# Kernel optimization log

Hardware: AMD Instinct MI355X
Metric: run time of the kernel (lower is better)

Reference implementation:

```python
import jax, jax.numpy as jnp
import numpy as np

N_USER = 100000
N_ITEM = 200000


def setup_inputs() -> dict:
    key = jax.random.key(0)
    ks = jax.random.split(key, 9)
    n = N_USER + N_ITEM
    nnz = 9600000
    return {
        "users_emb": jax.random.normal(ks[0], (N_USER, 64), dtype=jnp.float32) * 0.1,
        "items_emb": jax.random.normal(ks[1], (N_ITEM, 64), dtype=jnp.float32) * 0.1,
        "user_sim_neighbor": jax.random.randint(ks[2], (N_USER, 10), 0, N_USER),
        "user_sim_weight": jax.random.uniform(ks[3], (N_USER, 10), dtype=jnp.float32),
        "item_sim_neighbor": jax.random.randint(ks[4], (N_ITEM, 10), 0, N_ITEM),
        "item_sim_weight": jax.random.uniform(ks[5], (N_ITEM, 10), dtype=jnp.float32),
        "graph_rows": jax.random.randint(ks[6], (nnz,), 0, n),
        "graph_cols": jax.random.randint(ks[7], (nnz,), 0, n),
        "graph_vals": jax.random.uniform(ks[8], (nnz,), dtype=jnp.float32),
    }


def reference(users_emb, items_emb, user_sim_neighbor, user_sim_weight,
              item_sim_neighbor, item_sim_weight, graph_rows, graph_cols, graph_vals):
    n = users_emb.shape[0] + items_emb.shape[0]
    emb = jnp.concatenate([users_emb, items_emb], axis=0)  # [n, d]

    # top-k neighbor gather + weighted sum (users then items)
    user_neighbor_emb = jnp.einsum("nk,nkd->nd", user_sim_weight, users_emb[user_sim_neighbor])
    item_neighbor_emb = jnp.einsum("nk,nkd->nd", item_sim_weight, items_emb[item_sim_neighbor])
    neighbor_emb = jnp.concatenate([user_neighbor_emb, item_neighbor_emb], axis=0)

    # sparse graph matmul: all_emb = Graph @ emb  (COO rows/cols/vals)
    all_emb = jax.ops.segment_sum(graph_vals[:, None] * emb[graph_cols], graph_rows,
                                  num_segments=n)

    emb = emb + neighbor_emb + all_emb
    users = emb[:users_emb.shape[0]]
    items = emb[users_emb.shape[0]:]
    return users, items
```

## Files before the change

kernel.cpp:

```cpp
#include <hip/hip_runtime.h>

#define N_USER 100000
#define N_ITEM 200000
#define N_TOT  (N_USER + N_ITEM)
#define D      64
#define RPB    64
#define NB     ((N_TOT + RPB - 1) / RPB)
#define NBLK_F 512
#define THR_A  512
#define CAP    2304
#define SCAN_CHUNK 2048

__device__ __forceinline__ unsigned short f2bf(float f) {
    unsigned b = __float_as_uint(f);
    unsigned r = (b + 0x7FFFu + ((b >> 16) & 1u)) >> 16;
    return (unsigned short)r;
}
__device__ __forceinline__ float bf2f(unsigned short u) {
    return __uint_as_float(((unsigned)u) << 16);
}

__global__ __launch_bounds__(256) void conv_kernel(const float* __restrict__ users,
                                                   const float* __restrict__ items,
                                                   ushort* __restrict__ emb16) {
    size_t i = (size_t)blockIdx.x * blockDim.x + threadIdx.x;
    const size_t total = (size_t)N_TOT * D / 4;
    if (i >= total) return;
    size_t e0 = i * 4;
    const size_t usz = (size_t)N_USER * D;
    const float* src = (e0 < usz) ? users + e0 : items + (e0 - usz);
    float4 v = *reinterpret_cast<const float4*>(src);
    ushort4 o;
    o.x = f2bf(v.x); o.y = f2bf(v.y); o.z = f2bf(v.z); o.w = f2bf(v.w);
    *reinterpret_cast<ushort4*>(emb16 + e0) = o;
}


__global__ __launch_bounds__(THR_A) void count_fused(const int* __restrict__ rows,
                                                     int* __restrict__ tot, int nnz, int chunk) {
    __shared__ int h[NB];
    for (int k = threadIdx.x; k < NB; k += blockDim.x) h[k] = 0;
    __syncthreads();
    int lo = blockIdx.x * chunk;
    int hi = min(lo + chunk, nnz);
    for (int i = lo + threadIdx.x; i < hi; i += blockDim.x)
        atomicAdd(&h[rows[i] >> 6], 1);
    __syncthreads();
    for (int k = threadIdx.x; k < NB; k += blockDim.x)
        if (h[k]) atomicAdd(&tot[k], h[k]);
}

__global__ __launch_bounds__(1024) void scan_kernel(const int* __restrict__ tot,
                                                    int* __restrict__ bstart,
                                                    int* __restrict__ gcur, int nnz) {
    __shared__ int s[1024];
    const int t = threadIdx.x;
    const int PER = (NB + 1023) / 1024;
    int loc[8];
    int sum = 0;
    #pragma unroll
    for (int k = 0; k < PER; ++k) {
        int idx = t * PER + k;
        int v = (idx < NB) ? tot[idx] : 0;
        loc[k] = sum; sum += v;
    }
    s[t] = sum;
    __syncthreads();
    for (int off = 1; off < 1024; off <<= 1) {
        int v = (t >= off) ? s[t - off] : 0;
        __syncthreads();
        s[t] += v;
        __syncthreads();
    }
    int base = s[t] - sum;
    #pragma unroll
    for (int k = 0; k < PER; ++k) {
        int idx = t * PER + k;
        if (idx < NB) { bstart[idx] = base + loc[k]; gcur[idx] = base + loc[k]; }
    }
    if (t == 1023) bstart[NB] = nnz;
}

__global__ __launch_bounds__(THR_A) void fill_fused(const int* __restrict__ rows,
                                                    const int* __restrict__ cols,
                                                    const float* __restrict__ vals,
                                                    int* __restrict__ gcur,
                                                    uint2* __restrict__ eg, int nnz, int chunk) {
    __shared__ int h[NB];
    for (int k = threadIdx.x; k < NB; k += blockDim.x) h[k] = 0;
    __syncthreads();
    int lo = blockIdx.x * chunk;
    int hi = min(lo + chunk, nnz);
    for (int i = lo + threadIdx.x; i < hi; i += blockDim.x)
        atomicAdd(&h[rows[i] >> 6], 1);
    __syncthreads();
    for (int k = threadIdx.x; k < NB; k += blockDim.x)
        if (h[k]) h[k] = atomicAdd(&gcur[k], h[k]);
    __syncthreads();
    for (int i = lo + threadIdx.x; i < hi; i += blockDim.x) {
        int r = rows[i];
        int k = r >> 6;
        int slot = atomicAdd(&h[k], 1);
        uint2 p;
        p.x = ((unsigned)(r & 63) << 19) | (unsigned)cols[i];
        p.y = __float_as_uint(vals[i]);
        eg[slot] = p;
    }
}

__global__ __launch_bounds__(256) void sortgather_kernel(
    const ushort* __restrict__ emb16,
    const int*   __restrict__ unb,   const float* __restrict__ uw,
    const int*   __restrict__ inb,   const float* __restrict__ iw,
    const int*   __restrict__ bstart, const uint2* __restrict__ eg,
    float* __restrict__ out)
{
    __shared__ uint2 lds_e[CAP];
    __shared__ int h[RPB], st[RPB], cur[RPB];

    const int tid  = threadIdx.x;
    const int g    = tid >> 4;
    const int sub  = tid & 15;
    const int d0   = sub * 4;
    const int k    = blockIdx.x;
    const int row0 = k * RPB;

    float4 acc[4];
    #pragma unroll
    for (int rr = 0; rr < 4; ++rr) {
        const int row = row0 + rr * 16 + g;
        if (row >= N_TOT) { acc[rr] = make_float4(0.f, 0.f, 0.f, 0.f); continue; }
        ushort4 ub = *reinterpret_cast<const ushort4*>(emb16 + (size_t)row * D + d0);
        float4 a = make_float4(bf2f(ub.x), bf2f(ub.y), bf2f(ub.z), bf2f(ub.w));
        if (row < N_USER) {
            const int*   nb = unb + (size_t)row * 10;
            const float* w  = uw  + (size_t)row * 10;
            #pragma unroll
            for (int q = 0; q < 10; ++q) {
                ushort4 u = *reinterpret_cast<const ushort4*>(emb16 + (size_t)nb[q] * D + d0);
                float wq = w[q];
                a.x += wq * bf2f(u.x); a.y += wq * bf2f(u.y);
                a.z += wq * bf2f(u.z); a.w += wq * bf2f(u.w);
            }
        } else {
            const int r = row - N_USER;
            const int*   nb = inb + (size_t)r * 10;
            const float* w  = iw  + (size_t)r * 10;
            #pragma unroll
            for (int q = 0; q < 10; ++q) {
                ushort4 u = *reinterpret_cast<const ushort4*>(emb16 + ((size_t)nb[q] + N_USER) * D + d0);
                float wq = w[q];
                a.x += wq * bf2f(u.x); a.y += wq * bf2f(u.y);
                a.z += wq * bf2f(u.z); a.w += wq * bf2f(u.w);
            }
        }
        acc[rr] = a;
    }

    const int s = bstart[k];
    const int e = bstart[k + 1];

    for (int cs = s; cs < e; cs += CAP) {
        const int n = min(e - cs, CAP);

        if (tid < RPB) h[tid] = 0;
        __syncthreads();
        for (int i = tid; i < n; i += 256)
            atomicAdd(&h[eg[cs + i].x >> 19], 1);
        __syncthreads();
        if (tid < RPB) {
            int orig = h[tid];
            int v = orig;
            #pragma unroll
            for (int off = 1; off < RPB; off <<= 1) {
                int u = __shfl_up(v, off);
                if (tid >= off) v += u;
            }
            st[tid]  = v - orig;
            cur[tid] = v - orig;
        }
        __syncthreads();
        for (int i = tid; i < n; i += 256) {
            uint2 p = eg[cs + i];
            int slot = atomicAdd(&cur[p.x >> 19], 1);
            lds_e[slot] = p;
        }
        __syncthreads();

        #pragma unroll
        for (int rr = 0; rr < 4; ++rr) {
            const int r  = rr * 16 + g;
            const int b0 = st[r];
            const int cr = h[r];
            int j = 0;
            for (; j + 3 < cr; j += 4) {
                uint2 p0 = lds_e[b0 + j],     p1 = lds_e[b0 + j + 1];
                uint2 p2 = lds_e[b0 + j + 2], p3 = lds_e[b0 + j + 3];
                ushort4 u0 = *reinterpret_cast<const ushort4*>(emb16 + (size_t)(p0.x & 0x7FFFFu) * D + d0);
                ushort4 u1 = *reinterpret_cast<const ushort4*>(emb16 + (size_t)(p1.x & 0x7FFFFu) * D + d0);
                ushort4 u2 = *reinterpret_cast<const ushort4*>(emb16 + (size_t)(p2.x & 0x7FFFFu) * D + d0);
                ushort4 u3 = *reinterpret_cast<const ushort4*>(emb16 + (size_t)(p3.x & 0x7FFFFu) * D + d0);
                float a0 = __uint_as_float(p0.y), a1 = __uint_as_float(p1.y);
                float a2 = __uint_as_float(p2.y), a3 = __uint_as_float(p3.y);
                acc[rr].x += a0 * bf2f(u0.x); acc[rr].y += a0 * bf2f(u0.y);
                acc[rr].z += a0 * bf2f(u0.z); acc[rr].w += a0 * bf2f(u0.w);
                acc[rr].x += a1 * bf2f(u1.x); acc[rr].y += a1 * bf2f(u1.y);
                acc[rr].z += a1 * bf2f(u1.z); acc[rr].w += a1 * bf2f(u1.w);
                acc[rr].x += a2 * bf2f(u2.x); acc[rr].y += a2 * bf2f(u2.y);
                acc[rr].z += a2 * bf2f(u2.z); acc[rr].w += a2 * bf2f(u2.w);
                acc[rr].x += a3 * bf2f(u3.x); acc[rr].y += a3 * bf2f(u3.y);
                acc[rr].z += a3 * bf2f(u3.z); acc[rr].w += a3 * bf2f(u3.w);
            }
            for (; j < cr; ++j) {
                uint2 p = lds_e[b0 + j];
                ushort4 u = *reinterpret_cast<const ushort4*>(emb16 + (size_t)(p.x & 0x7FFFFu) * D + d0);
                float a = __uint_as_float(p.y);
                acc[rr].x += a * bf2f(u.x); acc[rr].y += a * bf2f(u.y);
                acc[rr].z += a * bf2f(u.z); acc[rr].w += a * bf2f(u.w);
            }
        }
        __syncthreads();
    }

    #pragma unroll
    for (int rr = 0; rr < 4; ++rr) {
        const int row = row0 + rr * 16 + g;
        if (row < N_TOT)
            *reinterpret_cast<float4*>(&out[(size_t)row * D + d0]) = acc[rr];
    }
}


__global__ void count_kernel(const int* __restrict__ rows, int* __restrict__ cnt, int nnz) {
    int i = blockIdx.x * blockDim.x + threadIdx.x;
    int stride = gridDim.x * blockDim.x;
    for (; i < nnz; i += stride) atomicAdd(&cnt[rows[i]], 1);
}

__global__ void scan_block_sums(const int* __restrict__ cnt, int* __restrict__ bsum, int n) {
    __shared__ int sdata[256];
    int base = blockIdx.x * SCAN_CHUNK;
    int s = 0;
    for (int t = threadIdx.x; t < SCAN_CHUNK; t += 256) {
        int idx = base + t;
        s += (idx < n) ? cnt[idx] : 0;
    }
    sdata[threadIdx.x] = s;
    __syncthreads();
    for (int off = 128; off > 0; off >>= 1) {
        if (threadIdx.x < off) sdata[threadIdx.x] += sdata[threadIdx.x + off];
        __syncthreads();
    }
    if (threadIdx.x == 0) bsum[blockIdx.x] = sdata[0];
}

__global__ void scan_bsum_kernel(int* __restrict__ bsum, int nb) {
    if (threadIdx.x == 0 && blockIdx.x == 0) {
        int acc = 0;
        for (int i = 0; i < nb; ++i) { int v = bsum[i]; bsum[i] = acc; acc += v; }
    }
}

__global__ void scan_final(const int* __restrict__ cnt, const int* __restrict__ bsum,
                           int* __restrict__ row_start, int n, int nnz) {
    __shared__ int sums[256];
    int b = blockIdx.x, t = threadIdx.x;
    int base = b * SCAN_CHUNK;
    int loc[8];
    int s = 0;
    #pragma unroll
    for (int k = 0; k < 8; ++k) {
        int idx = base + t * 8 + k;
        int v = (idx < n) ? cnt[idx] : 0;
        loc[k] = s; s += v;
    }
    sums[t] = s;
    __syncthreads();
    for (int off = 1; off < 256; off <<= 1) {
        int v = (t >= off) ? sums[t - off] : 0;
        __syncthreads();
        sums[t] += v;
        __syncthreads();
    }
    int off0 = bsum[b] + (sums[t] - s);
    #pragma unroll
    for (int k = 0; k < 8; ++k) {
        int idx = base + t * 8 + k;
        if (idx < n) row_start[idx] = off0 + loc[k];
    }
    if (b == gridDim.x - 1 && t == 255) row_start[n] = nnz;
}

__global__ void fill_kernel(const int* __restrict__ rows, const int* __restrict__ cols,
                            const float* __restrict__ vals, const int* __restrict__ row_start,
                            int* __restrict__ pos, uint2* __restrict__ eg, int nnz) {
    int i = blockIdx.x * blockDim.x + threadIdx.x;
    int stride = gridDim.x * blockDim.x;
    for (; i < nnz; i += stride) {
        int r = rows[i];
        int p = atomicAdd(&pos[r], 1);
        uint2 e;
        e.x = (unsigned)cols[i];
        e.y = __float_as_uint(vals[i]);
        eg[row_start[r] + p] = e;
    }
}

__global__ __launch_bounds__(256) void gather16_kernel(
    const float* __restrict__ users, const float* __restrict__ items,
    const int*   __restrict__ unb,   const float* __restrict__ uw,
    const int*   __restrict__ inb,   const float* __restrict__ iw,
    const int*   __restrict__ row_start, const uint2* __restrict__ eg,
    float* __restrict__ out)
{
    const int tid = threadIdx.x;
    const int grp = tid >> 4;
    const int sub = tid & 15;
    const int row = blockIdx.x * 16 + grp;
    if (row >= N_TOT) return;
    const int d0 = sub * 4;

    float4 acc;
    if (row < N_USER) {
        acc = *reinterpret_cast<const float4*>(&users[(size_t)row * D + d0]);
        const int*   nb = unb + (size_t)row * 10;
        const float* w  = uw  + (size_t)row * 10;
        #pragma unroll
        for (int q = 0; q < 10; ++q) {
            float4 v = *reinterpret_cast<const float4*>(&users[(size_t)nb[q] * D + d0]);
            float wq = w[q];
            acc.x += wq * v.x; acc.y += wq * v.y; acc.z += wq * v.z; acc.w += wq * v.w;
        }
    } else {
        int r = row - N_USER;
        acc = *reinterpret_cast<const float4*>(&items[(size_t)r * D + d0]);
        const int*   nb = inb + (size_t)r * 10;
        const float* w  = iw  + (size_t)r * 10;
        #pragma unroll
        for (int q = 0; q < 10; ++q) {
            float4 v = *reinterpret_cast<const float4*>(&items[(size_t)nb[q] * D + d0]);
            float wq = w[q];
            acc.x += wq * v.x; acc.y += wq * v.y; acc.z += wq * v.z; acc.w += wq * v.w;
        }
    }

    const int s = row_start[row];
    const int e = row_start[row + 1];
    int i = s;
    for (; i + 3 < e; i += 4) {
        uint2 p0 = eg[i], p1 = eg[i + 1], p2 = eg[i + 2], p3 = eg[i + 3];
        int c0 = (int)(p0.x & 0x7FFFFu), c1 = (int)(p1.x & 0x7FFFFu);
        int c2 = (int)(p2.x & 0x7FFFFu), c3 = (int)(p3.x & 0x7FFFFu);
        const float* s0 = (c0 < N_USER) ? users + (size_t)c0 * D : items + (size_t)(c0 - N_USER) * D;
        const float* s1 = (c1 < N_USER) ? users + (size_t)c1 * D : items + (size_t)(c1 - N_USER) * D;
        const float* s2 = (c2 < N_USER) ? users + (size_t)c2 * D : items + (size_t)(c2 - N_USER) * D;
        const float* s3 = (c3 < N_USER) ? users + (size_t)c3 * D : items + (size_t)(c3 - N_USER) * D;
        float4 v0 = *reinterpret_cast<const float4*>(s0 + d0);
        float4 v1 = *reinterpret_cast<const float4*>(s1 + d0);
        float4 v2 = *reinterpret_cast<const float4*>(s2 + d0);
        float4 v3 = *reinterpret_cast<const float4*>(s3 + d0);
        float a0 = __uint_as_float(p0.y), a1 = __uint_as_float(p1.y);
        float a2 = __uint_as_float(p2.y), a3 = __uint_as_float(p3.y);
        acc.x += a0 * v0.x; acc.y += a0 * v0.y; acc.z += a0 * v0.z; acc.w += a0 * v0.w;
        acc.x += a1 * v1.x; acc.y += a1 * v1.y; acc.z += a1 * v1.z; acc.w += a1 * v1.w;
        acc.x += a2 * v2.x; acc.y += a2 * v2.y; acc.z += a2 * v2.z; acc.w += a2 * v2.w;
        acc.x += a3 * v3.x; acc.y += a3 * v3.y; acc.z += a3 * v3.z; acc.w += a3 * v3.w;
    }
    for (; i < e; ++i) {
        uint2 p = eg[i];
        int c = (int)(p.x & 0x7FFFFu);
        const float* src = (c < N_USER) ? users + (size_t)c * D : items + (size_t)(c - N_USER) * D;
        float4 v = *reinterpret_cast<const float4*>(src + d0);
        float a = __uint_as_float(p.y);
        acc.x += a * v.x; acc.y += a * v.y; acc.z += a * v.z; acc.w += a * v.w;
    }

    *reinterpret_cast<float4*>(&out[(size_t)row * D + d0]) = acc;
}

__global__ __launch_bounds__(256) void base_neighbor_kernel(
    const float* __restrict__ users, const float* __restrict__ items,
    const int*   __restrict__ unb,   const float* __restrict__ uw,
    const int*   __restrict__ inb,   const float* __restrict__ iw,
    float* __restrict__ out)
{
    int gtid = blockIdx.x * blockDim.x + threadIdx.x;
    int row  = gtid >> 6;
    int lane = gtid & 63;
    if (row >= N_TOT) return;
    float acc;
    if (row < N_USER) {
        acc = users[(size_t)row * D + lane];
        const int*   nb = unb + (size_t)row * 10;
        const float* w  = uw  + (size_t)row * 10;
        #pragma unroll
        for (int q = 0; q < 10; ++q) acc += w[q] * users[(size_t)nb[q] * D + lane];
    } else {
        int r = row - N_USER;
        acc = items[(size_t)r * D + lane];
        const int*   nb = inb + (size_t)r * 10;
        const float* w  = iw  + (size_t)r * 10;
        #pragma unroll
        for (int q = 0; q < 10; ++q) acc += w[q] * items[(size_t)nb[q] * D + lane];
    }
    out[(size_t)row * D + lane] = acc;
}

__global__ __launch_bounds__(256) void edge_scatter_kernel(
    const float* __restrict__ users, const float* __restrict__ items,
    const int*   __restrict__ rows,  const int* __restrict__ cols,
    const float* __restrict__ vals,
    float* __restrict__ out, int nnz)
{
    int gtid = blockIdx.x * blockDim.x + threadIdx.x;
    int e    = gtid >> 6;
    int lane = gtid & 63;
    if (e >= nnz) return;
    int   r = rows[e];
    int   c = cols[e];
    float v = vals[e];
    const float* src = (c < N_USER) ? (users + (size_t)c * D)
                                    : (items + (size_t)(c - N_USER) * D);
    atomicAdd(&out[(size_t)r * D + lane], v * src[lane]);
}

extern "C" void kernel_launch(void* const* d_in, const int* in_sizes, int n_in,
                              void* d_out, int out_size, void* d_ws, size_t ws_size,
                              hipStream_t stream) {
    const float* users = (const float*)d_in[0];
    const float* items = (const float*)d_in[1];
    const int*   unb   = (const int*)  d_in[2];
    const float* uw    = (const float*)d_in[3];
    const int*   inb   = (const int*)  d_in[4];
    const float* iw    = (const float*)d_in[5];
    const int*   grow  = (const int*)  d_in[6];
    const int*   gcol  = (const int*)  d_in[7];
    const float* gval  = (const float*)d_in[8];
    float* out = (float*)d_out;

    const int nnz = in_sizes[6];

    const size_t A = 255;
    const size_t sz_eg       = (((size_t)nnz * 8) + A) & ~A;
    const size_t sz_tot      = (((size_t)NB * 4) + A) & ~A;
    const size_t sz_bstart   = (((size_t)(NB + 1) * 4) + A) & ~A;
    const size_t sz_gcur     = (((size_t)NB * 4) + A) & ~A;
    const size_t sz_rowstart = (((size_t)(N_TOT + 1) * 4) + A) & ~A;
    const size_t sz_emb16    = (((size_t)N_TOT * D * 2) + A) & ~A;
    const size_t need0 = sz_eg + sz_tot + sz_bstart + sz_gcur + sz_emb16;

    const size_t sz_cnt  = (((size_t)N_TOT * 4) + A) & ~A;
    const int    nb2     = (N_TOT + SCAN_CHUNK - 1) / SCAN_CHUNK;
    const size_t sz_bsum = (((size_t)nb2 * 4) + A) & ~A;
    const size_t need2 = sz_eg + sz_rowstart + sz_cnt + sz_bsum;

    if (ws_size >= need0) {
        char* wsp = (char*)d_ws;
        uint2*  eg     = (uint2*)wsp;  wsp += sz_eg;
        int*    tot    = (int*)wsp;    wsp += sz_tot;
        int*    bstart = (int*)wsp;    wsp += sz_bstart;
        int*    gcur   = (int*)wsp;    wsp += sz_gcur;
        ushort* emb16  = (ushort*)wsp;

        const int chunk = (nnz + NBLK_F - 1) / NBLK_F;
        const int conv_grid = (int)(((size_t)N_TOT * D / 4 + 255) / 256);

        conv_kernel<<<conv_grid, 256, 0, stream>>>(users, items, emb16);
        hipMemsetAsync(tot, 0, (size_t)NB * 4, stream);
        count_fused<<<NBLK_F, THR_A, 0, stream>>>(grow, tot, nnz, chunk);
        scan_kernel<<<1, 1024, 0, stream>>>(tot, bstart, gcur, nnz);
        fill_fused<<<NBLK_F, THR_A, 0, stream>>>(grow, gcol, gval, gcur, eg, nnz, chunk);
        sortgather_kernel<<<NB, 256, 0, stream>>>(emb16, unb, uw, inb, iw,
                                                  bstart, eg, out);
    } else if (ws_size >= need2) {
        char* wsp = (char*)d_ws;
        uint2* eg        = (uint2*)wsp;  wsp += sz_eg;
        int*   row_start = (int*)wsp;    wsp += sz_rowstart;
        int*   cnt       = (int*)wsp;    wsp += sz_cnt;
        int*   bsum      = (int*)wsp;

        hipMemsetAsync(cnt, 0, (size_t)N_TOT * 4, stream);
        count_kernel<<<2048, 256, 0, stream>>>(grow, cnt, nnz);
        scan_block_sums<<<nb2, 256, 0, stream>>>(cnt, bsum, N_TOT);
        scan_bsum_kernel<<<1, 64, 0, stream>>>(bsum, nb2);
        scan_final<<<nb2, 256, 0, stream>>>(cnt, bsum, row_start, N_TOT, nnz);
        hipMemsetAsync(cnt, 0, (size_t)N_TOT * 4, stream);
        fill_kernel<<<2048, 256, 0, stream>>>(grow, gcol, gval, row_start, cnt, eg, nnz);
        const int g16_grid = (N_TOT + 15) / 16;
        gather16_kernel<<<g16_grid, 256, 0, stream>>>(users, items, unb, uw, inb, iw,
                                                      row_start, eg, out);
    } else {
        int grid = (int)(((long long)N_TOT * 64 + 255) / 256);
        base_neighbor_kernel<<<grid, 256, 0, stream>>>(users, items, unb, uw, inb, iw, out);
        long long ethreads = (long long)nnz * 64;
        long long egrid = (ethreads + 255) / 256;
        edge_scatter_kernel<<<(int)egrid, 256, 0, stream>>>(users, items, grow, gcol, gval, out, nnz);
    }
}
```

Baseline: 571.6 us.

## Replace global count/scan/fill with per-block local binning and segmented gather

Removes the global histogram, single-block scan, and global-atomic fill pass. Each of 256 partition blocks now bins its own chunk of edges locally and writes a per-block offset table S. The gather kernel then has each of its 256 threads read one partition's segment for that row block. This drops one full pass over rows plus the memset and scan launches. In exchange the gather reads are strided and serial per thread, and edges beyond CAP2 per row block are silently dropped instead of being processed in chunks, which risks wrong results if a block exceeds capacity.

```diff
diff --git a/kernel.cpp b/kernel.cpp
--- a/kernel.cpp
+++ b/kernel.cpp
@@ -6,9 +6,8 @@
 #define D      64
 #define RPB    64
 #define NB     ((N_TOT + RPB - 1) / RPB)
-#define NBLK_F 512
-#define THR_A  512
-#define CAP    2304
+#define NBLK_L 256
+#define CAP2   2560
 #define SCAN_CHUNK 2048
 
 __device__ __forceinline__ unsigned short f2bf(float f) {
@@ -35,76 +34,62 @@
     *reinterpret_cast<ushort4*>(emb16 + e0) = o;
 }
 
-
-__global__ __launch_bounds__(THR_A) void count_fused(const int* __restrict__ rows,
-                                                     int* __restrict__ tot, int nnz, int chunk) {
-    __shared__ int h[NB];
-    for (int k = threadIdx.x; k < NB; k += blockDim.x) h[k] = 0;
-    __syncthreads();
-    int lo = blockIdx.x * chunk;
-    int hi = min(lo + chunk, nnz);
-    for (int i = lo + threadIdx.x; i < hi; i += blockDim.x)
+__global__ __launch_bounds__(512) void local_bin(const int* __restrict__ rows,
+                                                 const int* __restrict__ cols,
+                                                 const float* __restrict__ vals,
+                                                 int* __restrict__ S,
+                                                 uint2* __restrict__ eg, int nnz, int chunk) {
+    __shared__ int h[NB + 1];
+    __shared__ int ps[512];
+    const int b   = blockIdx.x;
+    const int tid = threadIdx.x;
+    const int lo  = b * chunk;
+    const int hi  = min(lo + chunk, nnz);
+
+    for (int k = tid; k < NB + 1; k += 512) h[k] = 0;
+    __syncthreads();
+    for (int i = lo + tid; i < hi; i += 512)
         atomicAdd(&h[rows[i] >> 6], 1);
     __syncthreads();
-    for (int k = threadIdx.x; k < NB; k += blockDim.x)
-        if (h[k]) atomicAdd(&tot[k], h[k]);
-}
-
-__global__ __launch_bounds__(1024) void scan_kernel(const int* __restrict__ tot,
-                                                    int* __restrict__ bstart,
-                                                    int* __restrict__ gcur, int nnz) {
-    __shared__ int s[1024];
-    const int t = threadIdx.x;
-    const int PER = (NB + 1023) / 1024;
-    int loc[8];
+
+    const int SEG = (NB + 511) / 512;
+    int loc[10];
     int sum = 0;
     #pragma unroll
-    for (int k = 0; k < PER; ++k) {
-        int idx = t * PER + k;
-        int v = (idx < NB) ? tot[idx] : 0;
-        loc[k] = sum; sum += v;
-    }
-    s[t] = sum;
-    __syncthreads();
-    for (int off = 1; off < 1024; off <<= 1) {
-        int v = (t >= off) ? s[t - off] : 0;
+    for (int j = 0; j < SEG; ++j) {
+        int idx = tid * SEG + j;
+        int v = (idx < NB) ? h[idx] : 0;
+        loc[j] = sum; sum += v;
+    }
+    ps[tid] = sum;
+    __syncthreads();
+    for (int off = 1; off < 512; off <<= 1) {
+        int v = (tid >= off) ? ps[tid - off] : 0;
         __syncthreads();
-        s[t] += v;
+        ps[tid] += v;
         __syncthreads();
     }
-    int base = s[t] - sum;
-    #pragma unroll
-    for (int k = 0; k < PER; ++k) {
-        int idx = t * PER + k;
-        if (idx < NB) { bstart[idx] = base + loc[k]; gcur[idx] = base + loc[k]; }
-    }
-    if (t == 1023) bstart[NB] = nnz;
-}
-
-__global__ __launch_bounds__(THR_A) void fill_fused(const int* __restrict__ rows,
-                                                    const int* __restrict__ cols,
-                                                    const float* __restrict__ vals,
-                                                    int* __restrict__ gcur,
-                                                    uint2* __restrict__ eg, int nnz, int chunk) {
-    __shared__ int h[NB];
-    for (int k = threadIdx.x; k < NB; k += blockDim.x) h[k] = 0;
-    __syncthreads();
-    int lo = blockIdx.x * chunk;
-    int hi = min(lo + chunk, nnz);
-    for (int i = lo + threadIdx.x; i < hi; i += blockDim.x)
-        atomicAdd(&h[rows[i] >> 6], 1);
-    __syncthreads();
-    for (int k = threadIdx.x; k < NB; k += blockDim.x)
-        if (h[k]) h[k] = atomicAdd(&gcur[k], h[k]);
-    __syncthreads();
-    for (int i = lo + threadIdx.x; i < hi; i += blockDim.x) {
+    const int myb = ps[tid] - sum;
+    __syncthreads();
+    #pragma unroll
+    for (int j = 0; j < SEG; ++j) {
+        int idx = tid * SEG + j;
+        if (idx < NB) h[idx] = myb + loc[j];
+    }
+    if (tid == 511) h[NB] = myb + sum;
+    __syncthreads();
+
+    for (int k = tid; k < NB + 1; k += 512)
+        S[(size_t)b * (NB + 1) + k] = h[k];
+    __syncthreads();
+
+    for (int i = lo + tid; i < hi; i += 512) {
         int r = rows[i];
-        int k = r >> 6;
-        int slot = atomicAdd(&h[k], 1);
+        int slot = atomicAdd(&h[r >> 6], 1);
         uint2 p;
         p.x = ((unsigned)(r & 63) << 19) | (unsigned)cols[i];
         p.y = __float_as_uint(vals[i]);
-        eg[slot] = p;
+        eg[lo + slot] = p;
     }
 }
 
@@ -112,10 +97,10 @@
     const ushort* __restrict__ emb16,
     const int*   __restrict__ unb,   const float* __restrict__ uw,
     const int*   __restrict__ inb,   const float* __restrict__ iw,
-    const int*   __restrict__ bstart, const uint2* __restrict__ eg,
-    float* __restrict__ out)
+    const int*   __restrict__ S,     const uint2* __restrict__ eg,
+    float* __restrict__ out, int chunk)
 {
-    __shared__ uint2 lds_e[CAP];
+    __shared__ uint2 lds_e[CAP2];
     __shared__ int h[RPB], st[RPB], cur[RPB];
 
     const int tid  = threadIdx.x;
@@ -124,6 +109,16 @@
     const int d0   = sub * 4;
     const int k    = blockIdx.x;
     const int row0 = k * RPB;
+
+    const size_t sidx = (size_t)tid * (NB + 1) + k;
+    const int rs = S[sidx];
+    const int re = S[sidx + 1];
+    const size_t cbase = (size_t)tid * chunk;
+
+    if (tid < RPB) h[tid] = 0;
+    __syncthreads();
+    for (int i = rs; i < re; ++i)
+        atomicAdd(&h[eg[cbase + i].x >> 19], 1);
 
     float4 acc[4];
     #pragma unroll
@@ -156,70 +151,59 @@
         }
         acc[rr] = a;
     }
-
-    const int s = bstart[k];
-    const int e = bstart[k + 1];
-
-    for (int cs = s; cs < e; cs += CAP) {
-        const int n = min(e - cs, CAP);
-
-        if (tid < RPB) h[tid] = 0;
-        __syncthreads();
-        for (int i = tid; i < n; i += 256)
-            atomicAdd(&h[eg[cs + i].x >> 19], 1);
-        __syncthreads();
-        if (tid < RPB) {
-            int orig = h[tid];
-            int v = orig;
-            #pragma unroll
-            for (int off = 1; off < RPB; off <<= 1) {
-                int u = __shfl_up(v, off);
-                if (tid >= off) v += u;
-            }
-            st[tid]  = v - orig;
-            cur[tid] = v - orig;
-        }
-        __syncthreads();
-        for (int i = tid; i < n; i += 256) {
-            uint2 p = eg[cs + i];
-            int slot = atomicAdd(&cur[p.x >> 19], 1);
-            lds_e[slot] = p;
-        }
-        __syncthreads();
-
+    __syncthreads();
+
+    if (tid < RPB) {
+        int orig = h[tid];
+        int v = orig;
         #pragma unroll
-        for (int rr = 0; rr < 4; ++rr) {
-            const int r  = rr * 16 + g;
-            const int b0 = st[r];
-            const int cr = h[r];
-            int j = 0;
-            for (; j + 3 < cr; j += 4) {
-                uint2 p0 = lds_e[b0 + j],     p1 = lds_e[b0 + j + 1];
-                uint2 p2 = lds_e[b0 + j + 2], p3 = lds_e[b0 + j + 3];
-                ushort4 u0 = *reinterpret_cast<const ushort4*>(emb16 + (size_t)(p0.x & 0x7FFFFu) * D + d0);
-                ushort4 u1 = *reinterpret_cast<const ushort4*>(emb16 + (size_t)(p1.x & 0x7FFFFu) * D + d0);
-                ushort4 u2 = *reinterpret_cast<const ushort4*>(emb16 + (size_t)(p2.x & 0x7FFFFu) * D + d0);
-                ushort4 u3 = *reinterpret_cast<const ushort4*>(emb16 + (size_t)(p3.x & 0x7FFFFu) * D + d0);
-                float a0 = __uint_as_float(p0.y), a1 = __uint_as_float(p1.y);
-                float a2 = __uint_as_float(p2.y), a3 = __uint_as_float(p3.y);
-                acc[rr].x += a0 * bf2f(u0.x); acc[rr].y += a0 * bf2f(u0.y);
-                acc[rr].z += a0 * bf2f(u0.z); acc[rr].w += a0 * bf2f(u0.w);
-                acc[rr].x += a1 * bf2f(u1.x); acc[rr].y += a1 * bf2f(u1.y);
-                acc[rr].z += a1 * bf2f(u1.z); acc[rr].w += a1 * bf2f(u1.w);
-                acc[rr].x += a2 * bf2f(u2.x); acc[rr].y += a2 * bf2f(u2.y);
-                acc[rr].z += a2 * bf2f(u2.z); acc[rr].w += a2 * bf2f(u2.w);
-                acc[rr].x += a3 * bf2f(u3.x); acc[rr].y += a3 * bf2f(u3.y);
-                acc[rr].z += a3 * bf2f(u3.z); acc[rr].w += a3 * bf2f(u3.w);
-            }
-            for (; j < cr; ++j) {
-                uint2 p = lds_e[b0 + j];
-                ushort4 u = *reinterpret_cast<const ushort4*>(emb16 + (size_t)(p.x & 0x7FFFFu) * D + d0);
-                float a = __uint_as_float(p.y);
-                acc[rr].x += a * bf2f(u.x); acc[rr].y += a * bf2f(u.y);
-                acc[rr].z += a * bf2f(u.z); acc[rr].w += a * bf2f(u.w);
-            }
-        }
-        __syncthreads();
+        for (int off = 1; off < RPB; off <<= 1) {
+            int u = __shfl_up(v, off);
+            if (tid >= off) v += u;
+        }
+        st[tid]  = v - orig;
+        cur[tid] = v - orig;
+    }
+    __syncthreads();
+
+    for (int i = rs; i < re; ++i) {
+        uint2 p = eg[cbase + i];
+        int slot = atomicAdd(&cur[p.x >> 19], 1);
+        if (slot < CAP2) lds_e[slot] = p;
+    }
+    __syncthreads();
+
+    #pragma unroll
+    for (int rr = 0; rr < 4; ++rr) {
+        const int r  = rr * 16 + g;
+        const int b0 = st[r];
+        const int cr = h[r];
+        int j = 0;
+        for (; j + 3 < cr; j += 4) {
+            uint2 p0 = lds_e[b0 + j],     p1 = lds_e[b0 + j + 1];
+            uint2 p2 = lds_e[b0 + j + 2], p3 = lds_e[b0 + j + 3];
+            ushort4 u0 = *reinterpret_cast<const ushort4*>(emb16 + (size_t)(p0.x & 0x7FFFFu) * D + d0);
+            ushort4 u1 = *reinterpret_cast<const ushort4*>(emb16 + (size_t)(p1.x & 0x7FFFFu) * D + d0);
+            ushort4 u2 = *reinterpret_cast<const ushort4*>(emb16 + (size_t)(p2.x & 0x7FFFFu) * D + d0);
+            ushort4 u3 = *reinterpret_cast<const ushort4*>(emb16 + (size_t)(p3.x & 0x7FFFFu) * D + d0);
+            float a0 = __uint_as_float(p0.y), a1 = __uint_as_float(p1.y);
+            float a2 = __uint_as_float(p2.y), a3 = __uint_as_float(p3.y);
+            acc[rr].x += a0 * bf2f(u0.x); acc[rr].y += a0 * bf2f(u0.y);
+            acc[rr].z += a0 * bf2f(u0.z); acc[rr].w += a0 * bf2f(u0.w);
+            acc[rr].x += a1 * bf2f(u1.x); acc[rr].y += a1 * bf2f(u1.y);
+            acc[rr].z += a1 * bf2f(u1.z); acc[rr].w += a1 * bf2f(u1.w);
+            acc[rr].x += a2 * bf2f(u2.x); acc[rr].y += a2 * bf2f(u2.y);
+            acc[rr].z += a2 * bf2f(u2.z); acc[rr].w += a2 * bf2f(u2.w);
+            acc[rr].x += a3 * bf2f(u3.x); acc[rr].y += a3 * bf2f(u3.y);
+            acc[rr].z += a3 * bf2f(u3.z); acc[rr].w += a3 * bf2f(u3.w);
+        }
+        for (; j < cr; ++j) {
+            uint2 p = lds_e[b0 + j];
+            ushort4 u = *reinterpret_cast<const ushort4*>(emb16 + (size_t)(p.x & 0x7FFFFu) * D + d0);
+            float a = __uint_as_float(p.y);
+            acc[rr].x += a * bf2f(u.x); acc[rr].y += a * bf2f(u.y);
+            acc[rr].z += a * bf2f(u.z); acc[rr].w += a * bf2f(u.w);
+        }
     }
 
     #pragma unroll
@@ -442,12 +426,10 @@
 
     const size_t A = 255;
     const size_t sz_eg       = (((size_t)nnz * 8) + A) & ~A;
-    const size_t sz_tot      = (((size_t)NB * 4) + A) & ~A;
-    const size_t sz_bstart   = (((size_t)(NB + 1) * 4) + A) & ~A;
-    const size_t sz_gcur     = (((size_t)NB * 4) + A) & ~A;
+    const size_t sz_S        = (((size_t)NBLK_L * (NB + 1) * 4) + A) & ~A;
+    const size_t sz_emb16    = (((size_t)N_TOT * D * 2) + A) & ~A;
     const size_t sz_rowstart = (((size_t)(N_TOT + 1) * 4) + A) & ~A;
-    const size_t sz_emb16    = (((size_t)N_TOT * D * 2) + A) & ~A;
-    const size_t need0 = sz_eg + sz_tot + sz_bstart + sz_gcur + sz_emb16;
+    const size_t need0 = sz_eg + sz_S + sz_emb16;
 
     const size_t sz_cnt  = (((size_t)N_TOT * 4) + A) & ~A;
     const int    nb2     = (N_TOT + SCAN_CHUNK - 1) / SCAN_CHUNK;
@@ -456,22 +438,17 @@
 
     if (ws_size >= need0) {
         char* wsp = (char*)d_ws;
-        uint2*  eg     = (uint2*)wsp;  wsp += sz_eg;
-        int*    tot    = (int*)wsp;    wsp += sz_tot;
-        int*    bstart = (int*)wsp;    wsp += sz_bstart;
-        int*    gcur   = (int*)wsp;    wsp += sz_gcur;
-        ushort* emb16  = (ushort*)wsp;
-
-        const int chunk = (nnz + NBLK_F - 1) / NBLK_F;
+        uint2*  eg    = (uint2*)wsp;  wsp += sz_eg;
+        int*    S     = (int*)wsp;    wsp += sz_S;
+        ushort* emb16 = (ushort*)wsp;
+
+        const int chunk = (nnz + NBLK_L - 1) / NBLK_L;
         const int conv_grid = (int)(((size_t)N_TOT * D / 4 + 255) / 256);
 
         conv_kernel<<<conv_grid, 256, 0, stream>>>(users, items, emb16);
-        hipMemsetAsync(tot, 0, (size_t)NB * 4, stream);
-        count_fused<<<NBLK_F, THR_A, 0, stream>>>(grow, tot, nnz, chunk);
-        scan_kernel<<<1, 1024, 0, stream>>>(tot, bstart, gcur, nnz);
-        fill_fused<<<NBLK_F, THR_A, 0, stream>>>(grow, gcol, gval, gcur, eg, nnz, chunk);
+        local_bin<<<NBLK_L, 512, 0, stream>>>(grow, gcol, gval, S, eg, nnz, chunk);
         sortgather_kernel<<<NB, 256, 0, stream>>>(emb16, unb, uw, inb, iw,
-                                                  bstart, eg, out);
+                                                  S, eg, out, chunk);
     } else if (ws_size >= need2) {
         char* wsp = (char*)d_ws;
         uint2* eg        = (uint2*)wsp;  wsp += sz_eg;
```

Result: slower. 629.5 us (+10.1%).

## Replace single-pass 4688-bucket scatter with two-level radix binning

Applied to the files above, without the earlier changes.

The one-pass fill scattered edges into about 4.7k row-block buckets, so writes were poorly coalesced. It is replaced by two passes. First the edges are binned into about 74 super-buckets of 4096 rows, then each super-bucket is split into 64-row blocks by sliced blocks, which gives more local and coalesced writes. The cost is an extra read and write of the 9.6M-edge array, plus a second edge buffer in the workspace. The count kernel's block count is also halved, and the fallback gather loses its 4-way unroll.

```diff
diff --git a/kernel.cpp b/kernel.cpp
--- a/kernel.cpp
+++ b/kernel.cpp
@@ -6,8 +6,10 @@
 #define D      64
 #define RPB    64
 #define NB     ((N_TOT + RPB - 1) / RPB)
-#define NBLK_F 512
-#define THR_A  512
+#define NSB    ((NB + 63) / 64)
+#define SLICES 8
+#define NBLK_A 512
+#define NBLK_C 256
 #define CAP    2304
 #define SCAN_CHUNK 2048
 
@@ -35,24 +37,24 @@
     *reinterpret_cast<ushort4*>(emb16 + e0) = o;
 }
 
-
-__global__ __launch_bounds__(THR_A) void count_fused(const int* __restrict__ rows,
-                                                     int* __restrict__ tot, int nnz, int chunk) {
+__global__ __launch_bounds__(512) void count2_kernel(const int* __restrict__ rows,
+                                                     int* __restrict__ totB, int nnz, int chunk) {
     __shared__ int h[NB];
-    for (int k = threadIdx.x; k < NB; k += blockDim.x) h[k] = 0;
+    for (int k = threadIdx.x; k < NB; k += 512) h[k] = 0;
     __syncthreads();
     int lo = blockIdx.x * chunk;
     int hi = min(lo + chunk, nnz);
-    for (int i = lo + threadIdx.x; i < hi; i += blockDim.x)
+    for (int i = lo + threadIdx.x; i < hi; i += 512)
         atomicAdd(&h[rows[i] >> 6], 1);
     __syncthreads();
-    for (int k = threadIdx.x; k < NB; k += blockDim.x)
-        if (h[k]) atomicAdd(&tot[k], h[k]);
-}
-
-__global__ __launch_bounds__(1024) void scan_kernel(const int* __restrict__ tot,
+    for (int k = threadIdx.x; k < NB; k += 512)
+        if (h[k]) atomicAdd(&totB[k], h[k]);
+}
+
+__global__ __launch_bounds__(1024) void scan_kernel(const int* __restrict__ totB,
                                                     int* __restrict__ bstart,
-                                                    int* __restrict__ gcur, int nnz) {
+                                                    int* __restrict__ gcurB,
+                                                    int* __restrict__ gcurA, int nnz) {
     __shared__ int s[1024];
     const int t = threadIdx.x;
     const int PER = (NB + 1023) / 1024;
@@ -61,7 +63,7 @@
     #pragma unroll
     for (int k = 0; k < PER; ++k) {
         int idx = t * PER + k;
-        int v = (idx < NB) ? tot[idx] : 0;
+        int v = (idx < NB) ? totB[idx] : 0;
         loc[k] = sum; sum += v;
     }
     s[t] = sum;
@@ -76,35 +78,65 @@
     #pragma unroll
     for (int k = 0; k < PER; ++k) {
         int idx = t * PER + k;
-        if (idx < NB) { bstart[idx] = base + loc[k]; gcur[idx] = base + loc[k]; }
+        if (idx < NB) { bstart[idx] = base + loc[k]; gcurB[idx] = base + loc[k]; }
     }
     if (t == 1023) bstart[NB] = nnz;
-}
-
-__global__ __launch_bounds__(THR_A) void fill_fused(const int* __restrict__ rows,
-                                                    const int* __restrict__ cols,
-                                                    const float* __restrict__ vals,
-                                                    int* __restrict__ gcur,
-                                                    uint2* __restrict__ eg, int nnz, int chunk) {
-    __shared__ int h[NB];
-    for (int k = threadIdx.x; k < NB; k += blockDim.x) h[k] = 0;
+    __syncthreads();
+    if (t < NSB) gcurA[t] = bstart[t * 64];
+}
+
+__global__ __launch_bounds__(512) void binA_kernel(const int* __restrict__ rows,
+                                                   const int* __restrict__ cols,
+                                                   const float* __restrict__ vals,
+                                                   int* __restrict__ gcurA,
+                                                   uint2* __restrict__ eg1, int nnz, int chunk) {
+    __shared__ int h[NSB];
+    if (threadIdx.x < NSB) h[threadIdx.x] = 0;
     __syncthreads();
     int lo = blockIdx.x * chunk;
     int hi = min(lo + chunk, nnz);
-    for (int i = lo + threadIdx.x; i < hi; i += blockDim.x)
-        atomicAdd(&h[rows[i] >> 6], 1);
-    __syncthreads();
-    for (int k = threadIdx.x; k < NB; k += blockDim.x)
-        if (h[k]) h[k] = atomicAdd(&gcur[k], h[k]);
-    __syncthreads();
-    for (int i = lo + threadIdx.x; i < hi; i += blockDim.x) {
+    for (int i = lo + threadIdx.x; i < hi; i += 512)
+        atomicAdd(&h[rows[i] >> 12], 1);
+    __syncthreads();
+    if (threadIdx.x < NSB && h[threadIdx.x])
+        h[threadIdx.x] = atomicAdd(&gcurA[threadIdx.x], h[threadIdx.x]);
+    __syncthreads();
+    for (int i = lo + threadIdx.x; i < hi; i += 512) {
         int r = rows[i];
-        int k = r >> 6;
-        int slot = atomicAdd(&h[k], 1);
+        int slot = atomicAdd(&h[r >> 12], 1);
         uint2 p;
-        p.x = ((unsigned)(r & 63) << 19) | (unsigned)cols[i];
+        p.x = ((unsigned)(r & 4095) << 19) | (unsigned)cols[i];
         p.y = __float_as_uint(vals[i]);
-        eg[slot] = p;
+        eg1[slot] = p;
+    }
+}
+
+__global__ __launch_bounds__(512) void binB_kernel(const int* __restrict__ bstart,
+                                                   int* __restrict__ gcurB,
+                                                   const uint2* __restrict__ eg1,
+                                                   uint2* __restrict__ eg2) {
+    __shared__ int h[64];
+    const int sb    = blockIdx.x / SLICES;
+    const int slice = blockIdx.x % SLICES;
+    const int s0 = bstart[sb * 64];
+    const int e0 = bstart[min((sb + 1) * 64, NB)];
+    const int len = e0 - s0;
+    const int chunk = (len + SLICES - 1) / SLICES;
+    const int lo = s0 + slice * chunk;
+    const int hi = min(lo + chunk, e0);
+
+    if (threadIdx.x < 64) h[threadIdx.x] = 0;
+    __syncthreads();
+    for (int i = lo + threadIdx.x; i < hi; i += 512)
+        atomicAdd(&h[(eg1[i].x >> 25) & 63], 1);
+    __syncthreads();
+    if (threadIdx.x < 64 && h[threadIdx.x])
+        h[threadIdx.x] = atomicAdd(&gcurB[sb * 64 + threadIdx.x], h[threadIdx.x]);
+    __syncthreads();
+    for (int i = lo + threadIdx.x; i < hi; i += 512) {
+        uint2 p = eg1[i];
+        int slot = atomicAdd(&h[(p.x >> 25) & 63], 1);
+        eg2[slot] = p;
     }
 }
 
@@ -166,7 +198,7 @@
         if (tid < RPB) h[tid] = 0;
         __syncthreads();
         for (int i = tid; i < n; i += 256)
-            atomicAdd(&h[eg[cs + i].x >> 19], 1);
+            atomicAdd(&h[(eg[cs + i].x >> 19) & 63], 1);
         __syncthreads();
         if (tid < RPB) {
             int orig = h[tid];
@@ -182,7 +214,7 @@
         __syncthreads();
         for (int i = tid; i < n; i += 256) {
             uint2 p = eg[cs + i];
-            int slot = atomicAdd(&cur[p.x >> 19], 1);
+            int slot = atomicAdd(&cur[(p.x >> 19) & 63], 1);
             lds_e[slot] = p;
         }
         __syncthreads();
@@ -346,27 +378,7 @@
 
     const int s = row_start[row];
     const int e = row_start[row + 1];
-    int i = s;
-    for (; i + 3 < e; i += 4) {
-        uint2 p0 = eg[i], p1 = eg[i + 1], p2 = eg[i + 2], p3 = eg[i + 3];
-        int c0 = (int)(p0.x & 0x7FFFFu), c1 = (int)(p1.x & 0x7FFFFu);
-        int c2 = (int)(p2.x & 0x7FFFFu), c3 = (int)(p3.x & 0x7FFFFu);
-        const float* s0 = (c0 < N_USER) ? users + (size_t)c0 * D : items + (size_t)(c0 - N_USER) * D;
-        const float* s1 = (c1 < N_USER) ? users + (size_t)c1 * D : items + (size_t)(c1 - N_USER) * D;
-        const float* s2 = (c2 < N_USER) ? users + (size_t)c2 * D : items + (size_t)(c2 - N_USER) * D;
-        const float* s3 = (c3 < N_USER) ? users + (size_t)c3 * D : items + (size_t)(c3 - N_USER) * D;
-        float4 v0 = *reinterpret_cast<const float4*>(s0 + d0);
-        float4 v1 = *reinterpret_cast<const float4*>(s1 + d0);
-        float4 v2 = *reinterpret_cast<const float4*>(s2 + d0);
-        float4 v3 = *reinterpret_cast<const float4*>(s3 + d0);
-        float a0 = __uint_as_float(p0.y), a1 = __uint_as_float(p1.y);
-        float a2 = __uint_as_float(p2.y), a3 = __uint_as_float(p3.y);
-        acc.x += a0 * v0.x; acc.y += a0 * v0.y; acc.z += a0 * v0.z; acc.w += a0 * v0.w;
-        acc.x += a1 * v1.x; acc.y += a1 * v1.y; acc.z += a1 * v1.z; acc.w += a1 * v1.w;
-        acc.x += a2 * v2.x; acc.y += a2 * v2.y; acc.z += a2 * v2.z; acc.w += a2 * v2.w;
-        acc.x += a3 * v3.x; acc.y += a3 * v3.y; acc.z += a3 * v3.z; acc.w += a3 * v3.w;
-    }
-    for (; i < e; ++i) {
+    for (int i = s; i < e; ++i) {
         uint2 p = eg[i];
         int c = (int)(p.x & 0x7FFFFu);
         const float* src = (c < N_USER) ? users + (size_t)c * D : items + (size_t)(c - N_USER) * D;
@@ -442,12 +454,13 @@
 
     const size_t A = 255;
     const size_t sz_eg       = (((size_t)nnz * 8) + A) & ~A;
-    const size_t sz_tot      = (((size_t)NB * 4) + A) & ~A;
     const size_t sz_bstart   = (((size_t)(NB + 1) * 4) + A) & ~A;
-    const size_t sz_gcur     = (((size_t)NB * 4) + A) & ~A;
+    const size_t sz_gcurB    = (((size_t)NB * 4) + A) & ~A;
+    const size_t sz_gcurA    = (((size_t)NSB * 4) + A) & ~A;
+    const size_t sz_totB     = (((size_t)NB * 4) + A) & ~A;
+    const size_t sz_emb16    = (((size_t)N_TOT * D * 2) + A) & ~A;
     const size_t sz_rowstart = (((size_t)(N_TOT + 1) * 4) + A) & ~A;
-    const size_t sz_emb16    = (((size_t)N_TOT * D * 2) + A) & ~A;
-    const size_t need0 = sz_eg + sz_tot + sz_bstart + sz_gcur + sz_emb16;
+    const size_t need0 = 2 * sz_eg + sz_bstart + sz_gcurB + sz_gcurA + sz_totB + sz_emb16;
 
     const size_t sz_cnt  = (((size_t)N_TOT * 4) + A) & ~A;
     const int    nb2     = (N_TOT + SCAN_CHUNK - 1) / SCAN_CHUNK;
@@ -456,22 +469,26 @@
 
     if (ws_size >= need0) {
         char* wsp = (char*)d_ws;
-        uint2*  eg     = (uint2*)wsp;  wsp += sz_eg;
-        int*    tot    = (int*)wsp;    wsp += sz_tot;
+        uint2*  eg1    = (uint2*)wsp;  wsp += sz_eg;
+        uint2*  eg2    = (uint2*)wsp;  wsp += sz_eg;
         int*    bstart = (int*)wsp;    wsp += sz_bstart;
-        int*    gcur   = (int*)wsp;    wsp += sz_gcur;
+        int*    gcurB  = (int*)wsp;    wsp += sz_gcurB;
+        int*    gcurA  = (int*)wsp;    wsp += sz_gcurA;
+        int*    totB   = (int*)wsp;    wsp += sz_totB;
         ushort* emb16  = (ushort*)wsp;
 
-        const int chunk = (nnz + NBLK_F - 1) / NBLK_F;
+        const int chunkC = (nnz + NBLK_C - 1) / NBLK_C;
+        const int chunkA = (nnz + NBLK_A - 1) / NBLK_A;
         const int conv_grid = (int)(((size_t)N_TOT * D / 4 + 255) / 256);
 
         conv_kernel<<<conv_grid, 256, 0, stream>>>(users, items, emb16);
-        hipMemsetAsync(tot, 0, (size_t)NB * 4, stream);
-        count_fused<<<NBLK_F, THR_A, 0, stream>>>(grow, tot, nnz, chunk);
-        scan_kernel<<<1, 1024, 0, stream>>>(tot, bstart, gcur, nnz);
-        fill_fused<<<NBLK_F, THR_A, 0, stream>>>(grow, gcol, gval, gcur, eg, nnz, chunk);
+        hipMemsetAsync(totB, 0, (size_t)NB * 4, stream);
+        count2_kernel<<<NBLK_C, 512, 0, stream>>>(grow, totB, nnz, chunkC);
+        scan_kernel<<<1, 1024, 0, stream>>>(totB, bstart, gcurB, gcurA, nnz);
+        binA_kernel<<<NBLK_A, 512, 0, stream>>>(grow, gcol, gval, gcurA, eg1, nnz, chunkA);
+        binB_kernel<<<NSB * SLICES, 512, 0, stream>>>(bstart, gcurB, eg1, eg2);
         sortgather_kernel<<<NB, 256, 0, stream>>>(emb16, unb, uw, inb, iw,
-                                                  bstart, eg, out);
+                                                  bstart, eg2, out);
     } else if (ws_size >= need2) {
         char* wsp = (char*)d_ws;
         uint2* eg        = (uint2*)wsp;  wsp += sz_eg;
```

Measured after the change: 487.3 us. 1.17x faster.
